# Optimization experiments

Measured on AMD Instinct MI355X. Metric: run time of the kernel, lower is better.

The kernel has to match this reference:

```python
import jax, jax.numpy as jnp
import numpy as np

D = 512

def setup_inputs() -> dict:
    key = jax.random.key(0)
    ks = jax.random.split(key, 12)
    B, d, H, W = 128, D, 14, 14
    s = 1.0 / np.sqrt(d)
    s2 = 1.0 / np.sqrt(2 * d)
    return {
        "m_prev": jax.random.normal(ks[0], (B, d), dtype=jnp.float32),
        "KB": jax.random.normal(ks[1], (B, d, H, W), dtype=jnp.float32),
        "c_i": jax.random.normal(ks[2], (B, d), dtype=jnp.float32),
        # Linear params stored as [in, out] so y = x @ W + b
        "W_m": jax.random.uniform(ks[3], (d, d), jnp.float32, -s, s),
        "b_m": jax.random.uniform(ks[4], (d,), jnp.float32, -s, s),
        "W_kb": jax.random.uniform(ks[5], (d, d), jnp.float32, -s, s),
        "b_kb": jax.random.uniform(ks[6], (d,), jnp.float32, -s, s),
        "W_merge": jax.random.uniform(ks[7], (2 * d, d), jnp.float32, -s2, s2),
        "b_merge": jax.random.uniform(ks[8], (d,), jnp.float32, -s2, s2),
        "W_attn": jax.random.uniform(ks[9], (d, 1), jnp.float32, -s, s),
        "b_attn": jax.random.uniform(ks[10], (1,), jnp.float32, -s, s),
    }


def reference(m_prev, KB, c_i, W_m, b_m, W_kb, b_kb, W_merge, b_merge, W_attn, b_attn):
    # m_prev: [B, d], KB: [B, d, H, W], c_i: [B, d]
    B, d, H, W = KB.shape
    KB_hw = jnp.transpose(KB, (0, 2, 3, 1))            # [B, H, W, d]
    _m_prev = (m_prev @ W_m + b_m)[:, None, None, :]   # [B, 1, 1, d]
    _KB = KB_hw @ W_kb + b_kb                          # [B, H, W, d]
    I = _m_prev * _KB                                  # [B, H, W, d]
    # merge: [I; KB] @ W_merge split into two halves to avoid the concat
    _I = I @ W_merge[:d] + KB_hw @ W_merge[d:] + b_merge  # [B, H, W, d]
    I2 = c_i[:, None, None, :] * _I                    # [B, H, W, d]
    mv = I2 @ W_attn + b_attn                          # [B, H, W, 1]
    # weighted spatial sum: sum over H*W of mv * KB_hw -> [B, d]
    m_new = jnp.einsum("bhwo,bhwd->bd", mv, KB_hw)
    return m_new
```

## Files before the change

kernel.cpp:

```cpp
#include <hip/hip_runtime.h>

#define D   512
#define HW  196
#define NS  8


__global__ void k_stage1(const float* __restrict__ m_prev, const float* __restrict__ W_m,
                         const float* __restrict__ b_m, const float* __restrict__ c,
                         const float* __restrict__ W_attn, const float* __restrict__ W_merge,
                         float* __restrict__ p_part, float* __restrict__ t12_part) {
    const int bx = blockIdx.x;
    const int t  = threadIdx.x;
    __shared__ float xs[16][64];

    if (bx < 128) {
        const int jt = bx & 1, bt = (bx >> 1) & 7, kt = bx >> 4;
        const int j  = jt * 256 + t;
        const int b0 = bt * 16;
        const int k0 = kt * 64;
        for (int i = t; i < 16 * 64; i += 256)
            xs[i >> 6][i & 63] = m_prev[(b0 + (i >> 6)) * D + k0 + (i & 63)];
        __syncthreads();
        float acc[16];
        #pragma unroll
        for (int bb = 0; bb < 16; ++bb) acc[bb] = 0.f;
        for (int kk = 0; kk < 64; ++kk) {
            float wv = W_m[(k0 + kk) * D + j];
            #pragma unroll
            for (int bb = 0; bb < 16; ++bb) acc[bb] += xs[bb][kk] * wv;
        }
        const float bias = (kt == 0) ? b_m[j] : 0.f;
        #pragma unroll
        for (int bb = 0; bb < 16; ++bb)
            p_part[((size_t)kt * 128 + b0 + bb) * D + j] = acc[bb] + bias;
    } else {
        const int i2 = bx - 128;
        const int kkt = i2 & 3, bt = (i2 >> 2) & 7, jt = i2 >> 5;
        const int kk = kkt * 256 + t;
        const int b0 = bt * 16;
        const int j0 = jt * 64;
        for (int i = t; i < 16 * 64; i += 256) {
            int bb = i >> 6, jj = i & 63;
            xs[bb][jj] = c[(b0 + bb) * D + j0 + jj] * W_attn[j0 + jj];
        }
        __syncthreads();
        float acc[16];
        #pragma unroll
        for (int bb = 0; bb < 16; ++bb) acc[bb] = 0.f;
        const float4* wrow = (const float4*)&W_merge[(size_t)kk * D + j0];
        for (int q = 0; q < 16; ++q) {
            float4 w4 = wrow[q];
            #pragma unroll
            for (int bb = 0; bb < 16; ++bb)
                acc[bb] += xs[bb][4*q+0] * w4.x + xs[bb][4*q+1] * w4.y
                         + xs[bb][4*q+2] * w4.z + xs[bb][4*q+3] * w4.w;
        }
        #pragma unroll
        for (int bb = 0; bb < 16; ++bb)
            t12_part[((size_t)jt * 128 + b0 + bb) * 1024 + kk] = acc[bb];
    }
}

__global__ void k_stage2(const float* __restrict__ p_part, const float* __restrict__ t12_part,
                         const float* __restrict__ W_kb, const float* __restrict__ c,
                         const float* __restrict__ W_attn, const float* __restrict__ b_merge,
                         const float* __restrict__ b_kb, const float* __restrict__ b_attn,
                         float* __restrict__ w_part, float* __restrict__ beta) {
    const int bx = blockIdx.x;
    const int t  = threadIdx.x;
    __shared__ float rs[16][64];

    if (bx < 128) {
        const int kpt = bx & 1, bt = (bx >> 1) & 7, kt = bx >> 4;
        const int kp = kpt * 256 + t;
        const int b0 = bt * 16;
        const int k0 = kt * 64;
        for (int i = t; i < 16 * 64; i += 256) {
            int bb = i >> 6, kk = i & 63;
            int b = b0 + bb, k = k0 + kk;
            float pv = 0.f, tv = 0.f;
            #pragma unroll
            for (int s = 0; s < NS; ++s) {
                pv += p_part[((size_t)s * 128 + b) * D + k];
                tv += t12_part[((size_t)s * 128 + b) * 1024 + k];
            }
            rs[bb][kk] = pv * tv;
        }
        __syncthreads();
        float acc[16];
        #pragma unroll
        for (int bb = 0; bb < 16; ++bb) acc[bb] = 0.f;
        const float4* wrow = (const float4*)&W_kb[(size_t)kp * D + k0];
        for (int q = 0; q < 16; ++q) {
            float4 w4 = wrow[q];
            #pragma unroll
            for (int bb = 0; bb < 16; ++bb)
                acc[bb] += rs[bb][4*q+0] * w4.x + rs[bb][4*q+1] * w4.y
                         + rs[bb][4*q+2] * w4.z + rs[bb][4*q+3] * w4.w;
        }
        #pragma unroll
        for (int bb = 0; bb < 16; ++bb) {
            float extra = 0.f;
            if (kt == 0) {
                #pragma unroll
                for (int s = 0; s < NS; ++s)
                    extra += t12_part[((size_t)s * 128 + b0 + bb) * 1024 + 512 + kp];
            }
            w_part[((size_t)kt * 128 + b0 + bb) * D + kp] = acc[bb] + extra;
        }
    } else {
        const int b = bx - 128;
        float sum = 0.f;
        for (int j = t; j < D; j += 256) {
            float pv = 0.f, tv = 0.f;
            #pragma unroll
            for (int s = 0; s < NS; ++s) {
                pv += p_part[((size_t)s * 128 + b) * D + j];
                tv += t12_part[((size_t)s * 128 + b) * 1024 + j];
            }
            float u = c[b * D + j] * W_attn[j];
            sum += b_merge[j] * u + b_kb[j] * (pv * tv);
        }
        #pragma unroll
        for (int off = 32; off; off >>= 1) sum += __shfl_down(sum, off, 64);
        __shared__ float red[4];
        if ((t & 63) == 0) red[t >> 6] = sum;
        __syncthreads();
        if (t == 0) beta[b] = red[0] + red[1] + red[2] + red[3] + b_attn[0];
    }
}

__global__ void k_mv(const float* __restrict__ KB, const float* __restrict__ w_part,
                     const float* __restrict__ beta, float* __restrict__ mvp) {
    const int b  = blockIdx.x >> 2;
    const int ks = blockIdx.x & 3;
    const int t  = threadIdx.x;
    __shared__ float wl[128];
    if (t < 128) {
        float s = 0.f;
        #pragma unroll
        for (int q = 0; q < NS; ++q)
            s += w_part[((size_t)q * 128 + b) * D + ks * 128 + t];
        wl[t] = s;
    }
    __syncthreads();
    if (t < HW) {
        const float* kbp = KB + (size_t)b * D * HW + (size_t)ks * 128 * HW + t;
        float acc = (ks == 0) ? beta[b] : 0.f;
        #pragma unroll 8
        for (int k = 0; k < 128; ++k) acc += kbp[(size_t)k * HW] * wl[k];
        mvp[(b * 4 + ks) * HW + t] = acc;
    }
}

__global__ void k_mnew(const float* __restrict__ KB, const float* __restrict__ mvp,
                       float* __restrict__ out) {
    const int b  = blockIdx.x >> 1;
    const int kh = blockIdx.x & 1;
    const int t  = threadIdx.x;
    __shared__ float ml[HW];
    if (t < HW)
        ml[t] = mvp[(b * 4 + 0) * HW + t] + mvp[(b * 4 + 1) * HW + t]
              + mvp[(b * 4 + 2) * HW + t] + mvp[(b * 4 + 3) * HW + t];
    __syncthreads();
    const int k = kh * 256 + t;
    const float4* row = (const float4*)(KB + (size_t)b * D * HW + (size_t)k * HW);
    float acc = 0.f;
    #pragma unroll 7
    for (int h4 = 0; h4 < 49; ++h4) {
        float4 v = row[h4];
        acc += v.x * ml[4*h4+0] + v.y * ml[4*h4+1] + v.z * ml[4*h4+2] + v.w * ml[4*h4+3];
    }
    out[b * D + k] = acc;
}

extern "C" void kernel_launch(void* const* d_in, const int* in_sizes, int n_in,
                              void* d_out, int out_size, void* d_ws, size_t ws_size,
                              hipStream_t stream) {
    const float* m_prev  = (const float*)d_in[0];
    const float* KB      = (const float*)d_in[1];
    const float* c_i     = (const float*)d_in[2];
    const float* W_m     = (const float*)d_in[3];
    const float* b_m     = (const float*)d_in[4];
    const float* W_kb    = (const float*)d_in[5];
    const float* b_kb    = (const float*)d_in[6];
    const float* W_merge = (const float*)d_in[7];
    const float* b_merge = (const float*)d_in[8];
    const float* W_attn  = (const float*)d_in[9];
    const float* b_attn  = (const float*)d_in[10];
    float* out = (float*)d_out;

    float* ws       = (float*)d_ws;
    float* p_part   = ws;
    float* t12_part = ws + 524288;
    float* w_part   = ws + 1572864;
    float* beta     = ws + 2097152;
    float* mvp      = ws + 2097280;

    k_stage1<<<384, 256, 0, stream>>>(m_prev, W_m, b_m, c_i, W_attn, W_merge,
                                      p_part, t12_part);
    k_stage2<<<256, 256, 0, stream>>>(p_part, t12_part, W_kb, c_i, W_attn,
                                      b_merge, b_kb, b_attn, w_part, beta);
    k_mv  <<<512, 256, 0, stream>>>(KB, w_part, beta, mvp);
    k_mnew<<<256, 256, 0, stream>>>(KB, mvp, out);
}
```

Baseline: 50.08 us.

## Fuse beta, mv and m_new stages into one per-batch 1024-thread kernel

```diff
diff --git a/kernel.cpp b/kernel.cpp
--- a/kernel.cpp
+++ b/kernel.cpp
@@ -62,116 +62,121 @@
 }
 
 __global__ void k_stage2(const float* __restrict__ p_part, const float* __restrict__ t12_part,
-                         const float* __restrict__ W_kb, const float* __restrict__ c,
-                         const float* __restrict__ W_attn, const float* __restrict__ b_merge,
-                         const float* __restrict__ b_kb, const float* __restrict__ b_attn,
-                         float* __restrict__ w_part, float* __restrict__ beta) {
+                         const float* __restrict__ W_kb, float* __restrict__ w_part) {
     const int bx = blockIdx.x;
     const int t  = threadIdx.x;
     __shared__ float rs[16][64];
 
-    if (bx < 128) {
-        const int kpt = bx & 1, bt = (bx >> 1) & 7, kt = bx >> 4;
-        const int kp = kpt * 256 + t;
-        const int b0 = bt * 16;
-        const int k0 = kt * 64;
-        for (int i = t; i < 16 * 64; i += 256) {
-            int bb = i >> 6, kk = i & 63;
-            int b = b0 + bb, k = k0 + kk;
-            float pv = 0.f, tv = 0.f;
+    const int kpt = bx & 1, bt = (bx >> 1) & 7, kt = bx >> 4;
+    const int kp = kpt * 256 + t;
+    const int b0 = bt * 16;
+    const int k0 = kt * 64;
+    for (int i = t; i < 16 * 64; i += 256) {
+        int bb = i >> 6, kk = i & 63;
+        int b = b0 + bb, k = k0 + kk;
+        float pv = 0.f, tv = 0.f;
+        #pragma unroll
+        for (int s = 0; s < NS; ++s) {
+            pv += p_part[((size_t)s * 128 + b) * D + k];
+            tv += t12_part[((size_t)s * 128 + b) * 1024 + k];
+        }
+        rs[bb][kk] = pv * tv;
+    }
+    __syncthreads();
+    float acc[16];
+    #pragma unroll
+    for (int bb = 0; bb < 16; ++bb) acc[bb] = 0.f;
+    const float4* wrow = (const float4*)&W_kb[(size_t)kp * D + k0];
+    for (int q = 0; q < 16; ++q) {
+        float4 w4 = wrow[q];
+        #pragma unroll
+        for (int bb = 0; bb < 16; ++bb)
+            acc[bb] += rs[bb][4*q+0] * w4.x + rs[bb][4*q+1] * w4.y
+                     + rs[bb][4*q+2] * w4.z + rs[bb][4*q+3] * w4.w;
+    }
+    #pragma unroll
+    for (int bb = 0; bb < 16; ++bb) {
+        float extra = 0.f;
+        if (kt == 0) {
             #pragma unroll
-            for (int s = 0; s < NS; ++s) {
-                pv += p_part[((size_t)s * 128 + b) * D + k];
-                tv += t12_part[((size_t)s * 128 + b) * 1024 + k];
-            }
-            rs[bb][kk] = pv * tv;
-        }
-        __syncthreads();
-        float acc[16];
-        #pragma unroll
-        for (int bb = 0; bb < 16; ++bb) acc[bb] = 0.f;
-        const float4* wrow = (const float4*)&W_kb[(size_t)kp * D + k0];
-        for (int q = 0; q < 16; ++q) {
-            float4 w4 = wrow[q];
-            #pragma unroll
-            for (int bb = 0; bb < 16; ++bb)
-                acc[bb] += rs[bb][4*q+0] * w4.x + rs[bb][4*q+1] * w4.y
-                         + rs[bb][4*q+2] * w4.z + rs[bb][4*q+3] * w4.w;
-        }
-        #pragma unroll
-        for (int bb = 0; bb < 16; ++bb) {
-            float extra = 0.f;
-            if (kt == 0) {
-                #pragma unroll
-                for (int s = 0; s < NS; ++s)
-                    extra += t12_part[((size_t)s * 128 + b0 + bb) * 1024 + 512 + kp];
-            }
-            w_part[((size_t)kt * 128 + b0 + bb) * D + kp] = acc[bb] + extra;
-        }
+            for (int s = 0; s < NS; ++s)
+                extra += t12_part[((size_t)s * 128 + b0 + bb) * 1024 + 512 + kp];
+        }
+        w_part[((size_t)kt * 128 + b0 + bb) * D + kp] = acc[bb] + extra;
+    }
+}
+
+__global__ __launch_bounds__(1024) void k_c(const float* __restrict__ KB,
+                                            const float* __restrict__ w_part,
+                                            const float* __restrict__ p_part,
+                                            const float* __restrict__ t12_part,
+                                            const float* __restrict__ c,
+                                            const float* __restrict__ W_attn,
+                                            const float* __restrict__ b_merge,
+                                            const float* __restrict__ b_kb,
+                                            const float* __restrict__ b_attn,
+                                            float* __restrict__ out) {
+    const int b = blockIdx.x;
+    const int t = threadIdx.x;
+    __shared__ float w_s[512];
+    __shared__ float part[4][200];
+    __shared__ float mv_s[200];
+    __shared__ float outp[2][512];
+    __shared__ float redB[8];
+
+    if (t < 512) {
+        float s = 0.f;
+        #pragma unroll
+        for (int q = 0; q < NS; ++q) s += w_part[((size_t)q * 128 + b) * D + t];
+        w_s[t] = s;
     } else {
-        const int b = bx - 128;
-        float sum = 0.f;
-        for (int j = t; j < D; j += 256) {
-            float pv = 0.f, tv = 0.f;
-            #pragma unroll
-            for (int s = 0; s < NS; ++s) {
-                pv += p_part[((size_t)s * 128 + b) * D + j];
-                tv += t12_part[((size_t)s * 128 + b) * 1024 + j];
-            }
-            float u = c[b * D + j] * W_attn[j];
-            sum += b_merge[j] * u + b_kb[j] * (pv * tv);
-        }
-        #pragma unroll
-        for (int off = 32; off; off >>= 1) sum += __shfl_down(sum, off, 64);
-        __shared__ float red[4];
-        if ((t & 63) == 0) red[t >> 6] = sum;
-        __syncthreads();
-        if (t == 0) beta[b] = red[0] + red[1] + red[2] + red[3] + b_attn[0];
-    }
-}
-
-__global__ void k_mv(const float* __restrict__ KB, const float* __restrict__ w_part,
-                     const float* __restrict__ beta, float* __restrict__ mvp) {
-    const int b  = blockIdx.x >> 2;
-    const int ks = blockIdx.x & 3;
-    const int t  = threadIdx.x;
-    __shared__ float wl[128];
-    if (t < 128) {
-        float s = 0.f;
-        #pragma unroll
-        for (int q = 0; q < NS; ++q)
-            s += w_part[((size_t)q * 128 + b) * D + ks * 128 + t];
-        wl[t] = s;
+        const int j = t - 512;
+        float pv = 0.f, tv = 0.f;
+        #pragma unroll
+        for (int q = 0; q < NS; ++q) {
+            pv += p_part[((size_t)q * 128 + b) * D + j];
+            tv += t12_part[((size_t)q * 128 + b) * 1024 + j];
+        }
+        float u = c[b * D + j] * W_attn[j];
+        float contrib = b_merge[j] * u + b_kb[j] * (pv * tv);
+        #pragma unroll
+        for (int off = 32; off; off >>= 1) contrib += __shfl_down(contrib, off, 64);
+        if ((t & 63) == 0) redB[(t >> 6) - 8] = contrib;
+    }
+    __syncthreads();
+
+    {
+        const int ks = t >> 8, hw = t & 255;
+        if (hw < HW) {
+            const float* kbp = KB + (size_t)b * D * HW + (size_t)ks * 128 * HW + hw;
+            float acc = 0.f;
+            #pragma unroll 16
+            for (int k = 0; k < 128; ++k) acc += kbp[(size_t)k * HW] * w_s[ks * 128 + k];
+            part[ks][hw] = acc;
+        }
     }
     __syncthreads();
     if (t < HW) {
-        const float* kbp = KB + (size_t)b * D * HW + (size_t)ks * 128 * HW + t;
-        float acc = (ks == 0) ? beta[b] : 0.f;
-        #pragma unroll 8
-        for (int k = 0; k < 128; ++k) acc += kbp[(size_t)k * HW] * wl[k];
-        mvp[(b * 4 + ks) * HW + t] = acc;
-    }
-}
-
-__global__ void k_mnew(const float* __restrict__ KB, const float* __restrict__ mvp,
-                       float* __restrict__ out) {
-    const int b  = blockIdx.x >> 1;
-    const int kh = blockIdx.x & 1;
-    const int t  = threadIdx.x;
-    __shared__ float ml[HW];
-    if (t < HW)
-        ml[t] = mvp[(b * 4 + 0) * HW + t] + mvp[(b * 4 + 1) * HW + t]
-              + mvp[(b * 4 + 2) * HW + t] + mvp[(b * 4 + 3) * HW + t];
-    __syncthreads();
-    const int k = kh * 256 + t;
-    const float4* row = (const float4*)(KB + (size_t)b * D * HW + (size_t)k * HW);
-    float acc = 0.f;
-    #pragma unroll 7
-    for (int h4 = 0; h4 < 49; ++h4) {
-        float4 v = row[h4];
-        acc += v.x * ml[4*h4+0] + v.y * ml[4*h4+1] + v.z * ml[4*h4+2] + v.w * ml[4*h4+3];
-    }
-    out[b * D + k] = acc;
+        float beta = redB[0] + redB[1] + redB[2] + redB[3]
+                   + redB[4] + redB[5] + redB[6] + redB[7] + b_attn[0];
+        mv_s[t] = part[0][t] + part[1][t] + part[2][t] + part[3][t] + beta;
+    }
+    __syncthreads();
+
+    {
+        const int k = t & 511, half = t >> 9;
+        const float4* row = (const float4*)(KB + (size_t)b * D * HW + (size_t)k * HW);
+        float acc = 0.f;
+        const int h0 = half ? 25 : 0, h1 = half ? 49 : 25;
+        for (int h4 = h0; h4 < h1; ++h4) {
+            float4 v = row[h4];
+            acc += v.x * mv_s[4*h4+0] + v.y * mv_s[4*h4+1]
+                 + v.z * mv_s[4*h4+2] + v.w * mv_s[4*h4+3];
+        }
+        outp[half][k] = acc;
+    }
+    __syncthreads();
+    if (t < 512) out[(size_t)b * D + t] = outp[0][t] + outp[1][t];
 }
 
 extern "C" void kernel_launch(void* const* d_in, const int* in_sizes, int n_in,
@@ -194,13 +199,10 @@
     float* p_part   = ws;
     float* t12_part = ws + 524288;
     float* w_part   = ws + 1572864;
-    float* beta     = ws + 2097152;
-    float* mvp      = ws + 2097280;
 
     k_stage1<<<384, 256, 0, stream>>>(m_prev, W_m, b_m, c_i, W_attn, W_merge,
                                       p_part, t12_part);
-    k_stage2<<<256, 256, 0, stream>>>(p_part, t12_part, W_kb, c_i, W_attn,
-                                      b_merge, b_kb, b_attn, w_part, beta);
-    k_mv  <<<512, 256, 0, stream>>>(KB, w_part, beta, mvp);
-    k_mnew<<<256, 256, 0, stream>>>(KB, mvp, out);
-}
+    k_stage2<<<128, 256, 0, stream>>>(p_part, t12_part, W_kb, w_part);
+    k_c     <<<128, 1024, 0, stream>>>(KB, w_part, p_part, t12_part, c_i, W_attn,
+                                       b_merge, b_kb, b_attn, out);
+}
```

Result: slower. 72.98 us (+45.7%).

## Split KB reductions into more blocks and use wave-per-row dot products in m_new

Applied to the files above, without the earlier changes.

```diff
diff --git a/kernel.cpp b/kernel.cpp
--- a/kernel.cpp
+++ b/kernel.cpp
@@ -3,6 +3,7 @@
 #define D   512
 #define HW  196
 #define NS  8
+#define MS  16
 
 
 __global__ void k_stage1(const float* __restrict__ m_prev, const float* __restrict__ W_m,
@@ -131,47 +132,58 @@
 }
 
 __global__ void k_mv(const float* __restrict__ KB, const float* __restrict__ w_part,
-                     const float* __restrict__ beta, float* __restrict__ mvp) {
-    const int b  = blockIdx.x >> 2;
-    const int ks = blockIdx.x & 3;
-    const int t  = threadIdx.x;
-    __shared__ float wl[128];
-    if (t < 128) {
+                     float* __restrict__ mvp) {
+    const int b  = blockIdx.x >> 4;
+    const int ks = blockIdx.x & (MS - 1);
+    const int t  = threadIdx.x;
+    __shared__ float wl[32];
+    if (t < 32) {
         float s = 0.f;
         #pragma unroll
         for (int q = 0; q < NS; ++q)
-            s += w_part[((size_t)q * 128 + b) * D + ks * 128 + t];
+            s += w_part[((size_t)q * 128 + b) * D + ks * 32 + t];
         wl[t] = s;
     }
     __syncthreads();
     if (t < HW) {
-        const float* kbp = KB + (size_t)b * D * HW + (size_t)ks * 128 * HW + t;
-        float acc = (ks == 0) ? beta[b] : 0.f;
-        #pragma unroll 8
-        for (int k = 0; k < 128; ++k) acc += kbp[(size_t)k * HW] * wl[k];
-        mvp[(b * 4 + ks) * HW + t] = acc;
+        const float* kbp = KB + (size_t)b * D * HW + (size_t)ks * 32 * HW + t;
+        float acc = 0.f;
+        #pragma unroll
+        for (int k = 0; k < 32; ++k) acc += kbp[(size_t)k * HW] * wl[k];
+        mvp[((size_t)b * MS + ks) * HW + t] = acc;
     }
 }
 
 __global__ void k_mnew(const float* __restrict__ KB, const float* __restrict__ mvp,
-                       float* __restrict__ out) {
-    const int b  = blockIdx.x >> 1;
-    const int kh = blockIdx.x & 1;
-    const int t  = threadIdx.x;
-    __shared__ float ml[HW];
-    if (t < HW)
-        ml[t] = mvp[(b * 4 + 0) * HW + t] + mvp[(b * 4 + 1) * HW + t]
-              + mvp[(b * 4 + 2) * HW + t] + mvp[(b * 4 + 3) * HW + t];
+                       const float* __restrict__ beta, float* __restrict__ out) {
+    const int b  = blockIdx.x >> 4;
+    const int kt = blockIdx.x & 15;
+    const int t  = threadIdx.x;
+    const int wave = t >> 6, lane = t & 63;
+    __shared__ float4 mv4_s[49];
+
+    if (t < HW) {
+        float s = beta[b];
+        #pragma unroll
+        for (int q = 0; q < MS; ++q)
+            s += mvp[((size_t)b * MS + q) * HW + t];
+        ((float*)mv4_s)[t] = s;
+    }
     __syncthreads();
-    const int k = kh * 256 + t;
-    const float4* row = (const float4*)(KB + (size_t)b * D * HW + (size_t)k * HW);
-    float acc = 0.f;
-    #pragma unroll 7
-    for (int h4 = 0; h4 < 49; ++h4) {
-        float4 v = row[h4];
-        acc += v.x * ml[4*h4+0] + v.y * ml[4*h4+1] + v.z * ml[4*h4+2] + v.w * ml[4*h4+3];
-    }
-    out[b * D + k] = acc;
+
+    const float4 m4 = (lane < 49) ? mv4_s[lane] : make_float4(0.f, 0.f, 0.f, 0.f);
+    #pragma unroll
+    for (int i = 0; i < 8; ++i) {
+        const int k = kt * 32 + wave * 8 + i;
+        float p = 0.f;
+        if (lane < 49) {
+            float4 v = ((const float4*)(KB + ((size_t)b * D + k) * HW))[lane];
+            p = v.x * m4.x + v.y * m4.y + v.z * m4.z + v.w * m4.w;
+        }
+        #pragma unroll
+        for (int off = 32; off; off >>= 1) p += __shfl_xor(p, off, 64);
+        if (lane == 0) out[(size_t)b * D + k] = p;
+    }
 }
 
 extern "C" void kernel_launch(void* const* d_in, const int* in_sizes, int n_in,
@@ -201,6 +213,6 @@
                                       p_part, t12_part);
     k_stage2<<<256, 256, 0, stream>>>(p_part, t12_part, W_kb, c_i, W_attn,
                                       b_merge, b_kb, b_attn, w_part, beta);
-    k_mv  <<<512, 256, 0, stream>>>(KB, w_part, beta, mvp);
-    k_mnew<<<256, 256, 0, stream>>>(KB, mvp, out);
-}
+    k_mv  <<<2048, 256, 0, stream>>>(KB, w_part, mvp);
+    k_mnew<<<2048, 256, 0, stream>>>(KB, mvp, beta, out);
+}
```

Result: slower. 51.13 us (+2.1%).
